# Kernel tuning notes

Measured on AMD Instinct MI355X. Metric: run time of the kernel, lower is better.

Reference implementation:

```python
import jax, jax.numpy as jnp
import numpy as np

N, H, W = 2, 96, 96
HL, WL = 48, 48
NCLS = 59


def _bn_params(key, c):
    k1, k2, k3, k4 = jax.random.split(key, 4)
    g = jax.random.uniform(k1, (c,), minval=0.5, maxval=1.5)
    b = jax.random.normal(k2, (c,)) * 0.1
    m = jax.random.normal(k3, (c,)) * 0.1
    v = jax.random.uniform(k4, (c,), minval=0.5, maxval=1.5)
    return jnp.stack([g, b, m, v])  # [4, C]


def _conv_w(key, shape):
    fan_in = shape[1] * shape[2] * shape[3]
    return jax.random.normal(key, shape) / np.sqrt(fan_in)


def setup_inputs() -> dict:
    key = jax.random.key(0)
    ks = jax.random.split(key, 32)
    return {
        "c1": jax.random.normal(ks[0], (N, 256, H, W)),
        "c2": jax.random.normal(ks[1], (N, 512, HL, WL)),
        "x": jax.random.normal(ks[2], (N, 2048, HL, WL)),
        "w_r1": _conv_w(ks[3], (64, 256, 3, 3)), "bn_r1": _bn_params(ks[4], 64),
        "w_r2": _conv_w(ks[5], (64, 64, 3, 3)), "bn_r2": _bn_params(ks[6], 64),
        "w_r3": _conv_w(ks[7], (64, 512, 1, 1)), "bn_r3": _bn_params(ks[8], 64),
        "w_p1": _conv_w(ks[9], (512, 2048, 1, 1)), "bn_p1": _bn_params(ks[10], 512),
        "w_p2": _conv_w(ks[11], (512, 2048, 1, 1)), "bn_p2": _bn_params(ks[12], 512),
        "w_p3": _conv_w(ks[13], (512, 2048, 1, 1)), "bn_p3": _bn_params(ks[14], 512),
        "w_p4": _conv_w(ks[15], (512, 2048, 1, 1)), "bn_p4": _bn_params(ks[16], 512),
        "w_c5": _conv_w(ks[17], (512, 4096, 3, 3)), "bn_c5": _bn_params(ks[18], 512),
        "w_c6": _conv_w(ks[19], (NCLS, 512, 1, 1)),
        "b_c6": jax.random.normal(ks[20], (NCLS,)) * 0.01,
    }


def conv2d(x, w, padding=0, dilation=1):
    return jax.lax.conv_general_dilated(
        x, w, window_strides=(1, 1), padding=[(padding, padding)] * 2,
        rhs_dilation=(dilation, dilation),
        dimension_numbers=("NCHW", "OIHW", "NCHW"))


def bn(x, p, eps=1e-5):
    g, b, m, v = p[0], p[1], p[2], p[3]
    scale = g * jax.lax.rsqrt(v + eps)
    return (x - m[None, :, None, None]) * scale[None, :, None, None] + b[None, :, None, None]


def resize_bilinear_ac(x, oh, ow):
    # bilinear, align_corners=True (matches torch interpolate)
    n, c, h, w = x.shape
    def coords(inp, out):
        if inp == 1 or out == 1:
            return jnp.zeros((out,), jnp.float32)
        return jnp.arange(out, dtype=jnp.float32) * ((inp - 1) / (out - 1))
    ys, xs = coords(h, oh), coords(w, ow)
    y0 = jnp.clip(jnp.floor(ys).astype(jnp.int32), 0, h - 1)
    y1 = jnp.clip(y0 + 1, 0, h - 1)
    wy = (ys - y0)[None, None, :, None]
    x0 = jnp.clip(jnp.floor(xs).astype(jnp.int32), 0, w - 1)
    x1 = jnp.clip(x0 + 1, 0, w - 1)
    wx = (xs - x0)[None, None, :]
    g = x[:, :, y0, :] * (1.0 - wy) + x[:, :, y1, :] * wy  # [n,c,oh,w]
    return g[:, :, :, x0] * (1.0 - wx[:, None]) + g[:, :, :, x1] * wx[:, None]


def unfold3x3_d2(x):
    # torch unfold(kernel=3, dilation=2, padding=2, stride=1) -> [n,c,9,h*w]
    n, c, h, w = x.shape
    p = jnp.pad(x, ((0, 0), (0, 0), (2, 2), (2, 2)))
    pats = jnp.stack([p[:, :, dy:dy + h, dx:dx + w]
                      for dy in (0, 2, 4) for dx in (0, 2, 4)], axis=2)
    return pats.reshape(n, c, 9, h * w)


def adaptive_avg_pool(x, s):
    n, c, h, w = x.shape  # h, w divisible by s here
    return x.reshape(n, c, s, h // s, s, w // s).mean(axis=(3, 5))


def reference(c1, c2, x, w_r1, bn_r1, w_r2, bn_r2, w_r3, bn_r3,
              w_p1, bn_p1, w_p2, bn_p2, w_p3, bn_p3, w_p4, bn_p4,
              w_c5, bn_c5, w_c6, b_c6):
    n, _, h, w = c1.shape
    # refine(c1): two dilated 3x3 convs -> query features [n,64,h,w]
    r = jax.nn.relu(bn(conv2d(c1, w_r1, padding=2, dilation=2), bn_r1))
    r = jax.nn.relu(bn(conv2d(r, w_r2, padding=2, dilation=2), bn_r2))
    # c2 -> upsample -> refine2 (1x1) -> key features [n,64,h,w]
    c2u = resize_bilinear_ac(c2, h, w)
    c2r = jax.nn.relu(bn(conv2d(c2u, w_r3), bn_r3))
    uc2 = unfold3x3_d2(c2r)                       # [n,64,9,hw]
    q = r.reshape(n, 64, h * w)                   # [n,64,hw]
    energy = jnp.einsum("ncp,nckp->npk", q, uc2)  # [n,hw,9]
    att = jax.nn.softmax(energy, axis=-1)
    # conv5 = PyramidPooling + 3x3 conv(4096->512) + BN + ReLU
    xh, xw = x.shape[2], x.shape[3]
    feats = [x]
    for s, wp, bnp in ((1, w_p1, bn_p1), (2, w_p2, bn_p2), (3, w_p3, bn_p3), (6, w_p4, bn_p4)):
        p = jax.nn.relu(bn(conv2d(adaptive_avg_pool(x, s), wp), bnp))
        feats.append(resize_bilinear_ac(p, xh, xw))
    psp = jnp.concatenate(feats, axis=1)          # [n,4096,xh,xw]
    out = jax.nn.relu(bn(conv2d(psp, w_c5, padding=1, dilation=1), bn_c5))  # [n,512,xh,xw]
    out0 = resize_bilinear_ac(out, h, w)          # [n,512,h,w]
    uo = unfold3x3_d2(out0)                       # [n,512,9,hw]
    agg = jnp.einsum("npk,nckp->ncp", att, uo).reshape(n, 512, h, w)
    # conv6: Dropout2d in eval mode = identity, then 1x1 conv with bias
    return conv2d(agg, w_c6) + b_c6[None, :, None, None]
```

## Files before the change

### kernel.cpp

```cpp
#include <hip/hip_runtime.h>
#include <hip/hip_bf16.h>
#include <cstddef>
#include <cstdint>

typedef __hip_bfloat16 hbf;
typedef __bf16 bf16x8 __attribute__((ext_vector_type(8)));
typedef __bf16 bf16x4 __attribute__((ext_vector_type(4)));
typedef float f32x4 __attribute__((ext_vector_type(4)));

#define GLDS(gp, lp) __builtin_amdgcn_global_load_lds( \
    (const __attribute__((address_space(1))) void*)(gp), \
    (__attribute__((address_space(3))) void*)(lp), 16, 0, 0)

__device__ __forceinline__ void bn_coef(const float* __restrict__ p, int C, int c,
                                        float& s, float& t) {
    float g = p[c];
    float b = p[C + c];
    float m = p[2 * C + c];
    float v = p[3 * C + c];
    s = g * rsqrtf(v + 1e-5f);
    t = b - m * s;
}

__global__ void k_fill0(uint32_t* __restrict__ p, int n) {
    int i = blockIdx.x * blockDim.x + threadIdx.x;
    if (i < n) p[i] = 0u;
}

__global__ __launch_bounds__(256) void k_c1trans(const float* __restrict__ x,
                                                 hbf* __restrict__ c1t) {
    __shared__ float tbuf[32][33];
    const int p0 = blockIdx.x * 32, c0 = blockIdx.y * 32, n = blockIdx.z;
    const int tx = threadIdx.x, ty = threadIdx.y;
#pragma unroll
    for (int i = 0; i < 4; ++i) {
        int ci = c0 + ty * 4 + i;
        tbuf[ty * 4 + i][tx] = x[((size_t)(n * 256 + ci)) * 9216 + p0 + tx];
    }
    __syncthreads();
#pragma unroll
    for (int i = 0; i < 4; ++i) {
        int p = p0 + ty * 4 + i;
        int pp = (p / 96 + 2) * 100 + (p % 96) + 2;
        c1t[((size_t)(n * 10000 + pp)) * 256 + c0 + tx] = __float2bfloat16(tbuf[tx][ty * 4 + i]);
    }
}

__global__ __launch_bounds__(256) void k_wsmall(const float* __restrict__ w1,
                                                hbf* __restrict__ wt1,
                                                const float* __restrict__ w2,
                                                hbf* __restrict__ wt2) {
    int b = blockIdx.x;
    if (b < 64) {
        int idx = b * 256 + threadIdx.x;
        int co = idx >> 8, ci = idx & 255;
        const float* s = w1 + ((size_t)(co * 256 + ci)) * 9;
#pragma unroll
        for (int tap = 0; tap < 9; ++tap)
            wt1[((size_t)(tap * 64 + co)) * 256 + ci] = __float2bfloat16(s[tap]);
    } else {
        int idx = (b - 64) * 256 + threadIdx.x;
        int co = idx >> 6, ci = idx & 63;
        const float* s = w2 + ((size_t)(co * 64 + ci)) * 9;
#pragma unroll
        for (int tap = 0; tap < 9; ++tap)
            wt2[((size_t)(tap * 64 + co)) * 64 + ci] = __float2bfloat16(s[tap]);
    }
}

template <int CI>
__global__ __launch_bounds__(256) void k_dconv_mfma(const hbf* __restrict__ wt,
                                                    const hbf* __restrict__ it,
                                                    float* __restrict__ accout) {
    __shared__ hbf As[2][3][64 * 32];
    __shared__ hbf Bs[2][140 * 32];
    const int tid = threadIdx.x;
    const int l = tid & 63, w = tid >> 6;
    const int P0 = blockIdx.x * 128;
    const int g  = blockIdx.y;
    const int r0 = tid >> 2;
    const int swzk = ((tid & 3) ^ ((r0 >> 1) & 3)) * 8;

    const int n_i = P0 / 9216;
    const int pl0 = P0 - n_i * 9216;
    const int pp0 = (pl0 / 96 + 2) * 100 + (pl0 % 96) + 2;
    const ptrdiff_t browbase = (ptrdiff_t)n_i * 10000 + pp0 + (g - 1) * 200 - 2;

    const int wn = w * 32;
    int jb[2];
#pragma unroll
    for (int tj = 0; tj < 2; ++tj) {
        int pl_lane = pl0 + wn + tj * 16 + (l & 15);
        jb[tj] = ((pl_lane / 96 + 2) * 100 + (pl_lane % 96) + 2) - pp0;
    }
    const int slotA = ((l >> 4) ^ ((l >> 1) & 3)) * 8;

    f32x4 acc[4][2];
#pragma unroll
    for (int i = 0; i < 4; ++i)
#pragma unroll
        for (int j = 0; j < 2; ++j) acc[i][j] = {0.f, 0.f, 0.f, 0.f};

    const hbf* gA = wt + ((size_t)(g * 192 + r0)) * CI + swzk;
    const hbf* gB = it + (size_t)(browbase + r0) * CI + swzk;

#define STAGE_D(buf, k0) do {                                                  \
        hbf* ldsA_ = &As[buf][0][0] + w * 512;                                 \
        hbf* ldsB_ = &Bs[buf][0] + w * 512;                                    \
        _Pragma("unroll")                                                      \
        for (int t_ = 0; t_ < 3; ++t_)                                         \
            GLDS(gA + (size_t)t_ * 64 * CI + (k0), ldsA_ + t_ * 2048);         \
        GLDS(gB + (k0), ldsB_);                                                \
        GLDS(gB + (size_t)64 * CI + (k0), ldsB_ + 2048);                       \
        if (tid < 48)                                                          \
            GLDS(gB + (size_t)128 * CI + (k0), &Bs[buf][0] + 4096);            \
    } while (0)

    STAGE_D(0, 0);
    int cur = 0;
#pragma unroll 2
    for (int k0 = 0; k0 < CI; k0 += 32) {
        __syncthreads();
        if (k0 + 32 < CI) STAGE_D(cur ^ 1, k0 + 32);
#pragma unroll
        for (int t = 0; t < 3; ++t) {
            bf16x8 af[4], bfr[2];
#pragma unroll
            for (int ti = 0; ti < 4; ++ti)
                af[ti] = *(const bf16x8*)(&As[cur][t][(ti * 16 + (l & 15)) * 32 + slotA]);
#pragma unroll
            for (int tj = 0; tj < 2; ++tj) {
                const int brow = jb[tj] + 2 * t;
                bfr[tj] = *(const bf16x8*)(&Bs[cur][0] + brow * 32 + (((l >> 4) ^ ((brow >> 1) & 3)) * 8));
            }
#pragma unroll
            for (int ti = 0; ti < 4; ++ti)
#pragma unroll
                for (int tj = 0; tj < 2; ++tj)
                    acc[ti][tj] = __builtin_amdgcn_mfma_f32_16x16x32_bf16(
                        af[ti], bfr[tj], acc[ti][tj], 0, 0, 0);
        }
        cur ^= 1;
    }
#undef STAGE_D

#pragma unroll
    for (int ti = 0; ti < 4; ++ti) {
        const int mrow = ti * 16 + (l >> 4) * 4;
#pragma unroll
        for (int tj = 0; tj < 2; ++tj) {
            const int px = P0 + wn + tj * 16 + (l & 15);
            const int n2 = px / 9216, pl2 = px % 9216;
            float* dst = accout + ((size_t)(n2 * 64 + mrow)) * 9216 + pl2;
#pragma unroll
            for (int r = 0; r < 4; ++r)
                atomicAdd(dst + (size_t)r * 9216, acc[ti][tj][r]);
        }
    }
}

__global__ __launch_bounds__(256) void k_ep_r1(const float* __restrict__ acc,
                                               const float* __restrict__ bnp,
                                               hbf* __restrict__ r1t) {
    const int q = threadIdx.x >> 6;
    const int ln = threadIdx.x & 63;
    const int pi = blockIdx.x * 64 + ln;
    const int n = pi / 9216, pl = pi % 9216;
    const int pp = (pl / 96 + 2) * 100 + (pl % 96) + 2;
    hbf* dst = r1t + ((size_t)(n * 10000 + pp)) * 64 + q * 16;
    const float* src = acc + (size_t)(n * 64 + q * 16) * 9216 + pl;
#pragma unroll
    for (int i = 0; i < 16; ++i) {
        float s, t; bn_coef(bnp, 64, q * 16 + i, s, t);
        dst[i] = __float2bfloat16(fmaxf(fmaf(src[(size_t)i * 9216], s, t), 0.f));
    }
}

__global__ __launch_bounds__(192) void k_conv1x1_c2(const float* __restrict__ c2,
                                                    const float* __restrict__ w,
                                                    float* __restrict__ outacc) {
    const int x = threadIdx.x;
    const int y = blockIdx.y * 4 + threadIdx.y;
    const int n = blockIdx.z >> 2;
    const int ci0 = (blockIdx.z & 3) * 128;
    const int cg = blockIdx.x;
    const int p = y * 48 + x;
    float acc[8];
#pragma unroll
    for (int j = 0; j < 8; ++j) acc[j] = 0.f;
    for (int ci = ci0; ci < ci0 + 128; ++ci) {
        float iv = c2[(size_t)(n * 512 + ci) * 2304 + p];
#pragma unroll
        for (int j = 0; j < 8; ++j)
            acc[j] = fmaf(iv, w[(size_t)(cg * 8 + j) * 512 + ci], acc[j]);
    }
#pragma unroll
    for (int j = 0; j < 8; ++j)
        atomicAdd(&outacc[(size_t)(n * 64 + cg * 8 + j) * 2304 + p], acc[j]);
}

__global__ void k_up96(const float* __restrict__ src, float* __restrict__ dst,
                       int C, const float* __restrict__ bnp) {
    int idx = blockIdx.x * blockDim.x + threadIdx.x;
    int p = idx % 9216;
    int nc = idx / 9216;
    int c = nc % C;
    int y = p / 96, x = p % 96;
    int yn = y * 47, xn = x * 47;
    int y0 = yn / 95, x0 = xn / 95;
    float wy = (float)(yn - y0 * 95) * (1.f / 95.f);
    float wx = (float)(xn - x0 * 95) * (1.f / 95.f);
    int y1 = min(y0 + 1, 47), x1 = min(x0 + 1, 47);
    const float* sp = src + (size_t)nc * 2304;
    float v00 = sp[y0 * 48 + x0], v01 = sp[y0 * 48 + x1];
    float v10 = sp[y1 * 48 + x0], v11 = sp[y1 * 48 + x1];
    float v = (v00 * (1.f - wx) + v01 * wx) * (1.f - wy)
            + (v10 * (1.f - wx) + v11 * wx) * wy;
    if (bnp) {
        float s, t; bn_coef(bnp, C, c, s, t);
        v = fmaxf(fmaf(v, s, t), 0.f);
    }
    dst[idx] = v;
}

__global__ __launch_bounds__(256) void k_attention(const float* __restrict__ qa,
                                                   const float* __restrict__ bnp,
                                                   const float* __restrict__ kf,
                                                   float* __restrict__ att) {
    const int wv = threadIdx.x >> 6;
    const int ln = threadIdx.x & 63;
    const int p_abs = blockIdx.x * 64 + ln;
    const int n = p_abs / 9216, p = p_abs % 9216;
    const int y = p / 96, x = p % 96;
    const float* qb = qa + ((size_t)(n * 64 + wv * 16)) * 9216 + p;
    float qv[16];
#pragma unroll
    for (int c = 0; c < 16; ++c) {
        float s, t; bn_coef(bnp, 64, wv * 16 + c, s, t);
        qv[c] = fmaxf(fmaf(qb[(size_t)c * 9216], s, t), 0.f);
    }
    const float* kb = kf + ((size_t)(n * 64 + wv * 16)) * 9216;
    float e[9];
#pragma unroll
    for (int ky = 0; ky < 3; ++ky)
#pragma unroll
        for (int kx = 0; kx < 3; ++kx) {
            int yy = y + 2 * ky - 2, xx = x + 2 * kx - 2;
            float s = 0.f;
            if (yy >= 0 && yy < 96 && xx >= 0 && xx < 96) {
                const float* kp = kb + yy * 96 + xx;
#pragma unroll
                for (int c = 0; c < 16; ++c) s = fmaf(qv[c], kp[(size_t)c * 9216], s);
            }
            e[ky * 3 + kx] = s;
        }
    __shared__ float pe[9][4][64];
#pragma unroll
    for (int k = 0; k < 9; ++k) pe[k][wv][ln] = e[k];
    __syncthreads();
    if (threadIdx.x < 64) {
        float ee[9];
#pragma unroll
        for (int k = 0; k < 9; ++k)
            ee[k] = (pe[k][0][ln] + pe[k][1][ln]) + (pe[k][2][ln] + pe[k][3][ln]);
        float m = ee[0];
#pragma unroll
        for (int k = 1; k < 9; ++k) m = fmaxf(m, ee[k]);
        float sum = 0.f;
#pragma unroll
        for (int k = 0; k < 9; ++k) { ee[k] = __expf(ee[k] - m); sum += ee[k]; }
        float inv = 1.f / sum;
        float* ap = att + (size_t)p_abs * 9;
#pragma unroll
        for (int k = 0; k < 9; ++k) ap[k] = ee[k] * inv;
    }
}

__global__ __launch_bounds__(64) void k_pool(const float* __restrict__ xin,
                                             float* __restrict__ pooled) {
    int b = blockIdx.x;
    int t = threadIdx.x;
    __shared__ float cells[50];
    if (t < 50) cells[t] = 0.f;
    __syncthreads();
    float rs = 0.f;
    if (t < 48) {
        const f32x4* rowv = (const f32x4*)(xin + (size_t)b * 2304 + t * 48);
        float s6[6];
#pragma unroll
        for (int j = 0; j < 6; ++j) {
            f32x4 u = rowv[2 * j], v = rowv[2 * j + 1];
            s6[j] = ((u[0] + u[1]) + (u[2] + u[3])) + ((v[0] + v[1]) + (v[2] + v[3]));
        }
        float s3a = s6[0] + s6[1], s3b = s6[2] + s6[3], s3c = s6[4] + s6[5];
        float s2a = s3a + s6[2], s2b = s6[3] + s3c;
        rs = s2a + s2b;
        int r6 = t >> 3, r3 = t >> 4, r2 = t / 24;
        atomicAdd(&cells[14 + r6 * 6 + 0], s6[0]);
        atomicAdd(&cells[14 + r6 * 6 + 1], s6[1]);
        atomicAdd(&cells[14 + r6 * 6 + 2], s6[2]);
        atomicAdd(&cells[14 + r6 * 6 + 3], s6[3]);
        atomicAdd(&cells[14 + r6 * 6 + 4], s6[4]);
        atomicAdd(&cells[14 + r6 * 6 + 5], s6[5]);
        atomicAdd(&cells[5 + r3 * 3 + 0], s3a);
        atomicAdd(&cells[5 + r3 * 3 + 1], s3b);
        atomicAdd(&cells[5 + r3 * 3 + 2], s3c);
        atomicAdd(&cells[1 + r2 * 2 + 0], s2a);
        atomicAdd(&cells[1 + r2 * 2 + 1], s2b);
    }
#pragma unroll
    for (int off = 32; off > 0; off >>= 1) rs += __shfl_down(rs, off);
    if (t == 0) atomicAdd(&cells[0], rs);
    __syncthreads();
    if (t < 50) {
        float inv = (t == 0) ? (1.f / 2304.f)
                  : (t < 5)  ? (1.f / 576.f)
                  : (t < 14) ? (1.f / 256.f)
                             : (1.f / 64.f);
        pooled[((size_t)(b >> 11) * 50 + t) * 2048 + (b & 2047)] = cells[t] * inv;
    }
}

__global__ __launch_bounds__(64) void k_pconv2(const float* __restrict__ pooled_t,
        const float* __restrict__ wp1, const float* __restrict__ bn1,
        const float* __restrict__ wp2, const float* __restrict__ bn2,
        const float* __restrict__ wp3, const float* __restrict__ bn3,
        const float* __restrict__ wp4, const float* __restrict__ bn4,
        float* __restrict__ pconv) {
    const int co = blockIdx.x, n = blockIdx.y;
    const int t = threadIdx.x;
    const int cell = (t < 50) ? t : 49;
    const float* w; const float* bnp;
    if (cell == 0)      { w = wp1; bnp = bn1; }
    else if (cell < 5)  { w = wp2; bnp = bn2; }
    else if (cell < 14) { w = wp3; bnp = bn3; }
    else                { w = wp4; bnp = bn4; }
    const float* pin = pooled_t + ((size_t)n * 50 + cell) * 2048;
    const float* wr = w + (size_t)co * 2048;
    float a0 = 0.f, a1 = 0.f, a2 = 0.f, a3 = 0.f;
    for (int c = 0; c < 2048; c += 4) {
        f32x4 v = *(const f32x4*)(pin + c);
        f32x4 ww = *(const f32x4*)(wr + c);
        a0 = fmaf(v[0], ww[0], a0);
        a1 = fmaf(v[1], ww[1], a1);
        a2 = fmaf(v[2], ww[2], a2);
        a3 = fmaf(v[3], ww[3], a3);
    }
    float a = (a0 + a1) + (a2 + a3);
    float s, tt; bn_coef(bnp, 512, co, s, tt);
    if (t < 50)
        pconv[((size_t)n * 512 + co) * 50 + cell] = fmaxf(fmaf(a, s, tt), 0.f);
}

__global__ __launch_bounds__(256) void k_wtrans_all(const float* __restrict__ w5,
                                                    hbf* __restrict__ wt,
                                                    hbf* __restrict__ wpsp) {
    int b = blockIdx.x;
    if (b < 4096) {
        int idx = b * 256 + threadIdx.x;
        int co = idx >> 11, ci = idx & 2047;
        const float* s = w5 + ((size_t)co * 4096 + ci) * 9;
#pragma unroll
        for (int tap = 0; tap < 9; ++tap)
            wt[((size_t)(tap * 512 + co)) * 2048 + ci] = __float2bfloat16(s[tap]);
    } else {
        int r = b - 4096;
        const int co = (r & 7) * 64 + (threadIdx.x & 63);
        const int bb = (r >> 3) & 3;
        const int c0 = (r >> 5) * 64 + (threadIdx.x >> 6) * 16;
        for (int i = 0; i < 16; ++i) {
            int c = c0 + i;
            const float* s = w5 + ((size_t)co * 4096 + 2048 + bb * 512 + c) * 9;
#pragma unroll
            for (int tap = 0; tap < 9; ++tap)
                wpsp[(((size_t)(tap * 4 + bb) * 512) + c) * 512 + co] = __float2bfloat16(s[tap]);
        }
    }
}

__global__ __launch_bounds__(64) void k_computeM2(const hbf* __restrict__ wpsp,
                                                  const float* __restrict__ pconv,
                                                  float* __restrict__ M) {
    const int cog = blockIdx.x, tap = blockIdx.y;
    const int n = blockIdx.z / 7, chunk = blockIdx.z % 7;
    const int cell0_t[7] = {0, 1, 5, 14, 23, 32, 41};
    const int ncell_t[7] = {1, 4, 9, 9, 9, 9, 9};
    const int btab[7]    = {0, 1, 2, 3, 3, 3, 3};
    const int cell0 = cell0_t[chunk], nc = ncell_t[chunk], b = btab[chunk];
    const int co = cog * 64 + threadIdx.x;
    const hbf* wb = wpsp + ((size_t)(tap * 4 + b) * 512) * 512 + co;
    const float* pc = pconv + (size_t)n * 512 * 50 + cell0;
    float acc[9];
#pragma unroll
    for (int j = 0; j < 9; ++j) acc[j] = 0.f;
    for (int c = 0; c < 512; ++c) {
        float w = __bfloat162float(wb[(size_t)c * 512]);
#pragma unroll
        for (int j = 0; j < 9; ++j)
            acc[j] = fmaf(w, pc[c * 50 + j], acc[j]);
    }
    float* Mp = M + ((size_t)(n * 512 + co) * 9 + tap) * 50 + cell0;
    for (int j = 0; j < nc; ++j) Mp[j] = acc[j];
}

struct B4 { int c0, c1, c2, c3; float w0, w1, w2, w3; };
__device__ __forceinline__ B4 cell_interp(int yy, int xx, int s, int base) {
    int sm1 = s - 1;
    int yn = yy * sm1, xn = xx * sm1;
    int y0 = yn / 47, x0 = xn / 47;
    float wy = (float)(yn - y0 * 47) * (1.f / 47.f);
    float wx = (float)(xn - x0 * 47) * (1.f / 47.f);
    int y1 = min(y0 + 1, sm1), x1 = min(x0 + 1, sm1);
    B4 r;
    r.c0 = base + y0 * s + x0; r.c1 = base + y0 * s + x1;
    r.c2 = base + y1 * s + x0; r.c3 = base + y1 * s + x1;
    r.w0 = (1.f - wy) * (1.f - wx); r.w1 = (1.f - wy) * wx;
    r.w2 = wy * (1.f - wx);         r.w3 = wy * wx;
    return r;
}

__global__ __launch_bounds__(256) void k_xtrans(const float* __restrict__ x,
                                                hbf* __restrict__ xtp) {
    __shared__ float tbuf[32][33];
    const int p0 = blockIdx.x * 32, c0 = blockIdx.y * 32, n = blockIdx.z;
    const int tx = threadIdx.x, ty = threadIdx.y;
#pragma unroll
    for (int i = 0; i < 4; ++i) {
        int ci = c0 + ty * 4 + i;
        tbuf[ty * 4 + i][tx] = x[((size_t)(n * 2048 + ci)) * 2304 + p0 + tx];
    }
    __syncthreads();
#pragma unroll
    for (int i = 0; i < 4; ++i) {
        int p = p0 + ty * 4 + i;
        int pp = (p / 48 + 1) * 50 + (p % 48) + 1;
        xtp[((size_t)(n * 2500 + pp)) * 2048 + c0 + tx] = __float2bfloat16(tbuf[tx][ty * 4 + i]);
    }
}

__global__ __launch_bounds__(256) void k_conv5_mfma(const hbf* __restrict__ wt,
                                                    const hbf* __restrict__ xtp,
                                                    float* __restrict__ c5acc) {
    __shared__ hbf As[2][3][128 * 32];
    __shared__ hbf Bs[2][136 * 32];
    const int tid = threadIdx.x;
    const int l = tid & 63, w = tid >> 6;
    const int m0 = blockIdx.x * 128;
    const int P0 = blockIdx.y * 128;
    const int g  = blockIdx.z;
    const int n_img = P0 / 2304;
    const int pbase = P0 - n_img * 2304;
    const int r0 = tid >> 2;
    const int swzk = ((tid & 3) ^ ((r0 >> 1) & 3)) * 8;

    const int pp0 = pbase + 2 * (pbase / 48) + 51;
    const ptrdiff_t browbase = (ptrdiff_t)n_img * 2500 + pp0 + (g - 1) * 50 - 1;

    const int wm = (w & 1) * 64, wn = (w >> 1) * 64;
    int jb[4];
#pragma unroll
    for (int tj = 0; tj < 4; ++tj) {
        int p = pbase + wn + tj * 16 + (l & 15);
        jb[tj] = p + 2 * (p / 48) + 51 - pp0;
    }
    const int slotA = ((l >> 4) ^ ((l >> 1) & 3)) * 8;

    f32x4 acc[4][4];
#pragma unroll
    for (int i = 0; i < 4; ++i)
#pragma unroll
        for (int j = 0; j < 4; ++j) acc[i][j] = {0.f, 0.f, 0.f, 0.f};

    const hbf* gA = wt + ((size_t)(g * 1536 + m0 + r0)) * 2048 + swzk;
    const hbf* gB = xtp + (size_t)(browbase + r0) * 2048 + swzk;

#define STAGE5(buf, k0) do {                                                       \
        hbf* ldsA_ = &As[buf][0][0] + w * 512;                                     \
        hbf* ldsB_ = &Bs[buf][0] + w * 512;                                        \
        _Pragma("unroll")                                                          \
        for (int t_ = 0; t_ < 3; ++t_) {                                           \
            GLDS(gA + (size_t)t_ * 512 * 2048 + (k0),             ldsA_ + t_ * 4096);      \
            GLDS(gA + (size_t)t_ * 512 * 2048 + 64 * 2048 + (k0), ldsA_ + t_ * 4096 + 2048); \
        }                                                                          \
        GLDS(gB + (k0),                      ldsB_);                               \
        GLDS(gB + (size_t)64 * 2048 + (k0),  ldsB_ + 2048);                        \
        if (tid < 32)                                                              \
            GLDS(gB + (size_t)128 * 2048 + (k0), &Bs[buf][0] + 4096);              \
    } while (0)

    STAGE5(0, 0);
    int cur = 0;
#pragma unroll 2
    for (int k0 = 0; k0 < 2048; k0 += 32) {
        __syncthreads();
        if (k0 + 32 < 2048) STAGE5(cur ^ 1, k0 + 32);
#pragma unroll
        for (int t = 0; t < 3; ++t) {
            bf16x8 af[4], bfr[4];
#pragma unroll
            for (int ti = 0; ti < 4; ++ti)
                af[ti] = *(const bf16x8*)(&As[cur][t][(wm + ti * 16 + (l & 15)) * 32 + slotA]);
#pragma unroll
            for (int tj = 0; tj < 4; ++tj) {
                const int brow = jb[tj] + t;
                bfr[tj] = *(const bf16x8*)(&Bs[cur][0] + brow * 32 + (((l >> 4) ^ ((brow >> 1) & 3)) * 8));
            }
#pragma unroll
            for (int ti = 0; ti < 4; ++ti)
#pragma unroll
                for (int tj = 0; tj < 4; ++tj)
                    acc[ti][tj] = __builtin_amdgcn_mfma_f32_16x16x32_bf16(
                        af[ti], bfr[tj], acc[ti][tj], 0, 0, 0);
        }
        cur ^= 1;
    }
#undef STAGE5

#pragma unroll
    for (int ti = 0; ti < 4; ++ti) {
        const int mrow = wm + ti * 16 + (l >> 4) * 4;
#pragma unroll
        for (int tj = 0; tj < 4; ++tj) {
            const int p = pbase + wn + tj * 16 + (l & 15);
            float* dst = c5acc + ((size_t)(n_img * 512 + m0 + mrow)) * 2304 + p;
#pragma unroll
            for (int r = 0; r < 4; ++r)
                atomicAdd(dst + (size_t)r * 2304, acc[ti][tj][r]);
        }
    }
}

__global__ __launch_bounds__(256) void k_bnrelu_psp(const float* __restrict__ c5acc,
                                                    const float* __restrict__ M,
                                                    const float* __restrict__ bnp,
                                                    hbf* __restrict__ c5out) {
    const int co = blockIdx.x, n = blockIdx.y;
    __shared__ float Ms[450];
    const float* Mrow = M + ((size_t)(n * 512 + co)) * 450;
    for (int i = threadIdx.x; i < 450; i += 256) Ms[i] = Mrow[i];
    __syncthreads();
    float s, t; bn_coef(bnp, 512, co, s, t);
    const size_t base = ((size_t)(n * 512 + co)) * 2304;
#pragma unroll
    for (int i = 0; i < 9; ++i) {
        int p = threadIdx.x + i * 256;
        int y = p / 48, x = p % 48;
        float a = c5acc[base + p];
#pragma unroll
        for (int ky = 0; ky < 3; ++ky) {
            int yy = y + ky - 1;
            if (yy < 0 || yy > 47) continue;
#pragma unroll
            for (int kx = 0; kx < 3; ++kx) {
                int xx = x + kx - 1;
                if (xx < 0 || xx > 47) continue;
                const float* Mp = Ms + (ky * 3 + kx) * 50;
                float sa = Mp[0];
                B4 b2 = cell_interp(yy, xx, 2, 1);
                B4 b3 = cell_interp(yy, xx, 3, 5);
                B4 b6 = cell_interp(yy, xx, 6, 14);
                sa = fmaf(b2.w0, Mp[b2.c0], sa); sa = fmaf(b2.w1, Mp[b2.c1], sa);
                sa = fmaf(b2.w2, Mp[b2.c2], sa); sa = fmaf(b2.w3, Mp[b2.c3], sa);
                sa = fmaf(b3.w0, Mp[b3.c0], sa); sa = fmaf(b3.w1, Mp[b3.c1], sa);
                sa = fmaf(b3.w2, Mp[b3.c2], sa); sa = fmaf(b3.w3, Mp[b3.c3], sa);
                sa = fmaf(b6.w0, Mp[b6.c0], sa); sa = fmaf(b6.w1, Mp[b6.c1], sa);
                sa = fmaf(b6.w2, Mp[b6.c2], sa); sa = fmaf(b6.w3, Mp[b6.c3], sa);
                a += sa;
            }
        }
        c5out[base + p] = __float2bfloat16(fmaxf(fmaf(a, s, t), 0.f));
    }
}

__global__ __launch_bounds__(192) void k_conv6s(const hbf* __restrict__ c5o,
                                                const float* __restrict__ w,
                                                float* __restrict__ out) {
    const int x = threadIdx.x;
    const int y = blockIdx.y * 4 + threadIdx.y;
    const int n = blockIdx.z;
    const int co = blockIdx.x;
    const int p = y * 48 + x;
    const hbf* ip = c5o + (size_t)n * 512 * 2304 + p;
    const float* wr = w + (size_t)co * 512;
    float a0 = 0.f, a1 = 0.f, a2 = 0.f, a3 = 0.f;
    for (int ci = 0; ci < 512; ci += 4) {
        a0 = fmaf(__bfloat162float(ip[(size_t)ci * 2304]),       wr[ci],     a0);
        a1 = fmaf(__bfloat162float(ip[(size_t)(ci + 1) * 2304]), wr[ci + 1], a1);
        a2 = fmaf(__bfloat162float(ip[(size_t)(ci + 2) * 2304]), wr[ci + 2], a2);
        a3 = fmaf(__bfloat162float(ip[(size_t)(ci + 3) * 2304]), wr[ci + 3], a3);
    }
    out[((size_t)n * 59 + co) * 2304 + p] = (a0 + a1) + (a2 + a3);
}

__global__ void k_final(const float* __restrict__ att, const float* __restrict__ c6s,
                        const float* __restrict__ bias, float* __restrict__ out) {
    int idx = blockIdx.x * blockDim.x + threadIdx.x;
    int p = idx % 9216;
    int nc = idx / 9216;
    int cls = nc % 59, n = nc / 59;
    int y = p / 96, x = p % 96;
    const float* ar = att + ((size_t)n * 9216 + p) * 9;
    const float* cp = c6s + (size_t)nc * 2304;
    int xs0[3], xs1[3], ys0[3], ys1[3];
    float fx[3], fy[3];
#pragma unroll
    for (int d = 0; d < 3; ++d) {
        int xx = x + 2 * d - 2;
        if (xx >= 0 && xx < 96) {
            int xn = xx * 47, x0 = xn / 95;
            xs0[d] = x0; xs1[d] = min(x0 + 1, 47);
            fx[d] = (float)(xn - x0 * 95) * (1.f / 95.f);
        } else { xs0[d] = -1; xs1[d] = 0; fx[d] = 0.f; }
        int yy = y + 2 * d - 2;
        if (yy >= 0 && yy < 96) {
            int yn = yy * 47, y0 = yn / 95;
            ys0[d] = y0; ys1[d] = min(y0 + 1, 47);
            fy[d] = (float)(yn - y0 * 95) * (1.f / 95.f);
        } else { ys0[d] = -1; ys1[d] = 0; fy[d] = 0.f; }
    }
    float a = bias[cls];
#pragma unroll
    for (int ky = 0; ky < 3; ++ky) {
        if (ys0[ky] < 0) continue;
        const float* r0 = cp + ys0[ky] * 48;
        const float* r1 = cp + ys1[ky] * 48;
        float wy = fy[ky];
#pragma unroll
        for (int kx = 0; kx < 3; ++kx) {
            if (xs0[kx] < 0) continue;
            float wx = fx[kx];
            float v0 = r0[xs0[kx]] * (1.f - wx) + r0[xs1[kx]] * wx;
            float v1 = r1[xs0[kx]] * (1.f - wx) + r1[xs1[kx]] * wx;
            a = fmaf(ar[ky * 3 + kx], v0 * (1.f - wy) + v1 * wy, a);
        }
    }
    out[idx] = a;
}

extern "C" void kernel_launch(void* const* d_in, const int* in_sizes, int n_in,
                              void* d_out, int out_size, void* d_ws, size_t ws_size,
                              hipStream_t stream) {
    const float* c1    = (const float*)d_in[0];
    const float* c2    = (const float*)d_in[1];
    const float* xin   = (const float*)d_in[2];
    const float* w_r1  = (const float*)d_in[3];
    const float* bn_r1 = (const float*)d_in[4];
    const float* w_r2  = (const float*)d_in[5];
    const float* bn_r2 = (const float*)d_in[6];
    const float* w_r3  = (const float*)d_in[7];
    const float* bn_r3 = (const float*)d_in[8];
    const float* w_p1  = (const float*)d_in[9];
    const float* bn_p1 = (const float*)d_in[10];
    const float* w_p2  = (const float*)d_in[11];
    const float* bn_p2 = (const float*)d_in[12];
    const float* w_p3  = (const float*)d_in[13];
    const float* bn_p3 = (const float*)d_in[14];
    const float* w_p4  = (const float*)d_in[15];
    const float* bn_p4 = (const float*)d_in[16];
    const float* w_c5  = (const float*)d_in[17];
    const float* bn_c5 = (const float*)d_in[18];
    const float* w_c6  = (const float*)d_in[19];
    const float* b_c6  = (const float*)d_in[20];
    float* out = (float*)d_out;
    (void)in_sizes; (void)n_in; (void)out_size; (void)ws_size;

    char* base = (char*)d_ws;
    float* att = (float*)base;
    char*  A   = base + 663552;
    hbf*   c1t   = (hbf*)A;
    hbf*   r1t   = (hbf*)(A + 10240000);
    float* r1acc = (float*)(A + 12800000);
    float* qacc  = (float*)(A + 17518592);
    float* c2acc = (float*)(A + 22237184);
    float* c2r   = (float*)(A + 28135424);
    hbf*   wr1t  = (hbf*)(A + 32854016);
    hbf*   wr2t  = (hbf*)(A + 33148928);
    hbf*   wpsp   = (hbf*)A;
    float* pooled = (float*)(A + 48791552);
    float* pconv  = (float*)(A + 49610752);
    float* M      = (float*)(A + 49815552);
    hbf*   xtp    = (hbf*)A;
    float* c5acc  = (float*)(A + 20480000);
    hbf*   wt     = (hbf*)(A + 29917184);
    hbf*   c5out = (hbf*)A;
    float* c6s   = (float*)(A + 4718592);

    k_fill0<<<dim3(22868), 256, 0, stream>>>((uint32_t*)A, 5854208);
    k_c1trans<<<dim3(288, 8, 2), dim3(32, 8), 0, stream>>>(c1, c1t);
    k_wsmall<<<dim3(80), 256, 0, stream>>>(w_r1, wr1t, w_r2, wr2t);
    k_dconv_mfma<256><<<dim3(144, 3), 256, 0, stream>>>(wr1t, c1t, r1acc);
    k_ep_r1<<<dim3(288), 256, 0, stream>>>(r1acc, bn_r1, r1t);
    k_dconv_mfma<64><<<dim3(144, 3), 256, 0, stream>>>(wr2t, r1t, qacc);
    k_conv1x1_c2<<<dim3(8, 12, 8), dim3(48, 4), 0, stream>>>(c2, w_r3, c2acc);
    k_up96<<<dim3(2 * 64 * 9216 / 256), 256, 0, stream>>>(c2acc, c2r, 64, bn_r3);
    k_attention<<<dim3(288), 256, 0, stream>>>(qacc, bn_r2, c2r, att);
    k_pool<<<dim3(4096), 64, 0, stream>>>(xin, pooled);
    k_pconv2<<<dim3(512, 2), 64, 0, stream>>>(pooled, w_p1, bn_p1, w_p2, bn_p2,
                                              w_p3, bn_p3, w_p4, bn_p4, pconv);
    k_wtrans_all<<<dim3(4352), 256, 0, stream>>>(w_c5, wt, wpsp);
    k_computeM2<<<dim3(8, 9, 14), 64, 0, stream>>>(wpsp, pconv, M);
    k_fill0<<<dim3(29216), 256, 0, stream>>>((uint32_t*)xtp, 7479296);
    k_xtrans<<<dim3(72, 64, 2), dim3(32, 8), 0, stream>>>(xin, xtp);
    k_conv5_mfma<<<dim3(4, 36, 3), 256, 0, stream>>>(wt, xtp, c5acc);
    k_bnrelu_psp<<<dim3(512, 2), 256, 0, stream>>>(c5acc, M, bn_c5, c5out);
    k_conv6s<<<dim3(59, 12, 2), dim3(48, 4), 0, stream>>>(c5out, w_c6, c6s);
    k_final<<<dim3(2 * 59 * 9216 / 256), 256, 0, stream>>>(att, c6s, b_c6, out);
}
```

Measured before the change: 661.7 us.

## Drop atomics in dilated conv and transpose attention inputs to pixel-major

The dilated 3x3 conv kernel now loops over all three kernel-row groups inside one block with 64-pixel tiles, so it writes results directly instead of accumulating through atomics. The zero-fill region shrinks to match. Two new transpose kernels apply BN/ReLU (and the bilinear upsample for the key features) and store q and k as pixel-major [p,64], so the attention kernel can use vectorized float4 loads instead of channel-strided ones. The c2 1x1 conv now computes 16 output channels per thread. The costs are two extra small kernels and a dconv grid with fewer blocks but longer serial K loops.

```diff
diff --git a/kernel.cpp b/kernel.cpp
--- a/kernel.cpp
+++ b/kernel.cpp
@@ -5,7 +5,6 @@
 
 typedef __hip_bfloat16 hbf;
 typedef __bf16 bf16x8 __attribute__((ext_vector_type(8)));
-typedef __bf16 bf16x4 __attribute__((ext_vector_type(4)));
 typedef float f32x4 __attribute__((ext_vector_type(4)));
 
 #define GLDS(gp, lp) __builtin_amdgcn_global_load_lds( \
@@ -72,90 +71,74 @@
 __global__ __launch_bounds__(256) void k_dconv_mfma(const hbf* __restrict__ wt,
                                                     const hbf* __restrict__ it,
                                                     float* __restrict__ accout) {
+    constexpr int KS = CI / 32;
     __shared__ hbf As[2][3][64 * 32];
-    __shared__ hbf Bs[2][140 * 32];
+    __shared__ hbf Bs[2][72 * 32];
     const int tid = threadIdx.x;
     const int l = tid & 63, w = tid >> 6;
-    const int P0 = blockIdx.x * 128;
-    const int g  = blockIdx.y;
+    const int P0 = blockIdx.x * 64;
     const int r0 = tid >> 2;
     const int swzk = ((tid & 3) ^ ((r0 >> 1) & 3)) * 8;
 
     const int n_i = P0 / 9216;
     const int pl0 = P0 - n_i * 9216;
     const int pp0 = (pl0 / 96 + 2) * 100 + (pl0 % 96) + 2;
-    const ptrdiff_t browbase = (ptrdiff_t)n_i * 10000 + pp0 + (g - 1) * 200 - 2;
-
-    const int wn = w * 32;
-    int jb[2];
-#pragma unroll
-    for (int tj = 0; tj < 2; ++tj) {
-        int pl_lane = pl0 + wn + tj * 16 + (l & 15);
-        jb[tj] = ((pl_lane / 96 + 2) * 100 + (pl_lane % 96) + 2) - pp0;
-    }
+    const ptrdiff_t bb0 = (ptrdiff_t)n_i * 10000 + pp0 - 202;
+
+    const int wn = w * 16;
+    const int pl_lane = pl0 + wn + (l & 15);
+    const int jb = ((pl_lane / 96 + 2) * 100 + (pl_lane % 96) + 2) - pp0;
     const int slotA = ((l >> 4) ^ ((l >> 1) & 3)) * 8;
 
-    f32x4 acc[4][2];
-#pragma unroll
-    for (int i = 0; i < 4; ++i)
-#pragma unroll
-        for (int j = 0; j < 2; ++j) acc[i][j] = {0.f, 0.f, 0.f, 0.f};
-
-    const hbf* gA = wt + ((size_t)(g * 192 + r0)) * CI + swzk;
-    const hbf* gB = it + (size_t)(browbase + r0) * CI + swzk;
-
-#define STAGE_D(buf, k0) do {                                                  \
+    f32x4 acc[4];
+#pragma unroll
+    for (int i = 0; i < 4; ++i) acc[i] = {0.f, 0.f, 0.f, 0.f};
+
+#define STAGE_D(buf, gg, k0) do {                                              \
+        const hbf* gA_ = wt + ((size_t)((gg) * 192 + r0)) * CI + swzk;         \
+        const hbf* gB_ = it + (size_t)(bb0 + (gg) * 200 + r0) * CI + swzk;     \
         hbf* ldsA_ = &As[buf][0][0] + w * 512;                                 \
         hbf* ldsB_ = &Bs[buf][0] + w * 512;                                    \
         _Pragma("unroll")                                                      \
         for (int t_ = 0; t_ < 3; ++t_)                                         \
-            GLDS(gA + (size_t)t_ * 64 * CI + (k0), ldsA_ + t_ * 2048);         \
-        GLDS(gB + (k0), ldsB_);                                                \
-        GLDS(gB + (size_t)64 * CI + (k0), ldsB_ + 2048);                       \
-        if (tid < 48)                                                          \
-            GLDS(gB + (size_t)128 * CI + (k0), &Bs[buf][0] + 4096);            \
+            GLDS(gA_ + (size_t)t_ * 64 * CI + (k0), ldsA_ + t_ * 2048);        \
+        GLDS(gB_ + (k0), ldsB_);                                               \
+        if (tid < 32)                                                          \
+            GLDS(gB_ + (size_t)64 * CI + (k0), &Bs[buf][0] + 2048);            \
     } while (0)
 
-    STAGE_D(0, 0);
+    STAGE_D(0, 0, 0);
     int cur = 0;
-#pragma unroll 2
-    for (int k0 = 0; k0 < CI; k0 += 32) {
-        __syncthreads();
-        if (k0 + 32 < CI) STAGE_D(cur ^ 1, k0 + 32);
-#pragma unroll
-        for (int t = 0; t < 3; ++t) {
-            bf16x8 af[4], bfr[2];
-#pragma unroll
-            for (int ti = 0; ti < 4; ++ti)
-                af[ti] = *(const bf16x8*)(&As[cur][t][(ti * 16 + (l & 15)) * 32 + slotA]);
-#pragma unroll
-            for (int tj = 0; tj < 2; ++tj) {
-                const int brow = jb[tj] + 2 * t;
-                bfr[tj] = *(const bf16x8*)(&Bs[cur][0] + brow * 32 + (((l >> 4) ^ ((brow >> 1) & 3)) * 8));
+    for (int g = 0; g < 3; ++g) {
+#pragma unroll
+        for (int ks = 0; ks < KS; ++ks) {
+            __syncthreads();
+            int ns = g * KS + ks + 1;
+            if (ns < 3 * KS) STAGE_D(cur ^ 1, ns / KS, (ns % KS) * 32);
+#pragma unroll
+            for (int t = 0; t < 3; ++t) {
+                const int brow = jb + 2 * t;
+                bf16x8 bfr = *(const bf16x8*)(&Bs[cur][0] + brow * 32 + (((l >> 4) ^ ((brow >> 1) & 3)) * 8));
+#pragma unroll
+                for (int ti = 0; ti < 4; ++ti) {
+                    bf16x8 af = *(const bf16x8*)(&As[cur][t][(ti * 16 + (l & 15)) * 32 + slotA]);
+                    acc[ti] = __builtin_amdgcn_mfma_f32_16x16x32_bf16(af, bfr, acc[ti], 0, 0, 0);
+                }
             }
-#pragma unroll
-            for (int ti = 0; ti < 4; ++ti)
-#pragma unroll
-                for (int tj = 0; tj < 2; ++tj)
-                    acc[ti][tj] = __builtin_amdgcn_mfma_f32_16x16x32_bf16(
-                        af[ti], bfr[tj], acc[ti][tj], 0, 0, 0);
-        }
-        cur ^= 1;
+            cur ^= 1;
+        }
     }
 #undef STAGE_D
 
+    const int px = P0 + wn + (l & 15);
+    const int n2 = px / 9216, pl2 = px % 9216;
 #pragma unroll
     for (int ti = 0; ti < 4; ++ti) {
         const int mrow = ti * 16 + (l >> 4) * 4;
-#pragma unroll
-        for (int tj = 0; tj < 2; ++tj) {
-            const int px = P0 + wn + tj * 16 + (l & 15);
-            const int n2 = px / 9216, pl2 = px % 9216;
-            float* dst = accout + ((size_t)(n2 * 64 + mrow)) * 9216 + pl2;
-#pragma unroll
-            for (int r = 0; r < 4; ++r)
-                atomicAdd(dst + (size_t)r * 9216, acc[ti][tj][r]);
-        }
+        float* dst = accout + ((size_t)(n2 * 64 + mrow)) * 9216 + pl2;
+#pragma unroll
+        for (int r = 0; r < 4; ++r)
+            dst[(size_t)r * 9216] = acc[ti][r];
     }
 }
 
@@ -176,6 +159,59 @@
     }
 }
 
+__global__ __launch_bounds__(256) void k_qt(const float* __restrict__ acc,
+                                            const float* __restrict__ bnp,
+                                            float* __restrict__ qt) {
+    __shared__ float tbuf[32][33];
+    const int p0 = blockIdx.x * 32, c0 = blockIdx.y * 32, n = blockIdx.z;
+    const int tx = threadIdx.x, ty = threadIdx.y;
+#pragma unroll
+    for (int i = 0; i < 4; ++i) {
+        int ci = c0 + ty * 4 + i;
+        tbuf[ty * 4 + i][tx] = acc[((size_t)(n * 64 + ci)) * 9216 + p0 + tx];
+    }
+    __syncthreads();
+    float s, t; bn_coef(bnp, 64, c0 + tx, s, t);
+#pragma unroll
+    for (int i = 0; i < 4; ++i) {
+        int p = p0 + ty * 4 + i;
+        qt[((size_t)(n * 9216 + p)) * 64 + c0 + tx] =
+            fmaxf(fmaf(tbuf[tx][ty * 4 + i], s, t), 0.f);
+    }
+}
+
+__global__ __launch_bounds__(256) void k_kt(const float* __restrict__ c2acc,
+                                            const float* __restrict__ bnp,
+                                            float* __restrict__ kt) {
+    __shared__ float tbuf[32][33];
+    const int p0 = blockIdx.x * 32, c0 = blockIdx.y * 32, n = blockIdx.z;
+    const int tx = threadIdx.x, ty = threadIdx.y;
+    const int p = p0 + tx;
+    const int y = p / 96, x = p % 96;
+    int yn = y * 47, xn = x * 47;
+    int y0 = yn / 95, x0 = xn / 95;
+    float wy = (float)(yn - y0 * 95) * (1.f / 95.f);
+    float wx = (float)(xn - x0 * 95) * (1.f / 95.f);
+    int y1 = min(y0 + 1, 47), x1 = min(x0 + 1, 47);
+#pragma unroll
+    for (int i = 0; i < 4; ++i) {
+        int c = c0 + ty * 4 + i;
+        const float* sp = c2acc + ((size_t)(n * 64 + c)) * 2304;
+        float v00 = sp[y0 * 48 + x0], v01 = sp[y0 * 48 + x1];
+        float v10 = sp[y1 * 48 + x0], v11 = sp[y1 * 48 + x1];
+        tbuf[ty * 4 + i][tx] = (v00 * (1.f - wx) + v01 * wx) * (1.f - wy)
+                             + (v10 * (1.f - wx) + v11 * wx) * wy;
+    }
+    __syncthreads();
+    float s, t; bn_coef(bnp, 64, c0 + tx, s, t);
+#pragma unroll
+    for (int i = 0; i < 4; ++i) {
+        int pw = p0 + ty * 4 + i;
+        kt[((size_t)(n * 9216 + pw)) * 64 + c0 + tx] =
+            fmaxf(fmaf(tbuf[tx][ty * 4 + i], s, t), 0.f);
+    }
+}
+
 __global__ __launch_bounds__(192) void k_conv1x1_c2(const float* __restrict__ c2,
                                                     const float* __restrict__ w,
                                                     float* __restrict__ outacc) {
@@ -185,61 +221,39 @@
     const int ci0 = (blockIdx.z & 3) * 128;
     const int cg = blockIdx.x;
     const int p = y * 48 + x;
-    float acc[8];
-#pragma unroll
-    for (int j = 0; j < 8; ++j) acc[j] = 0.f;
+    float acc[16];
+#pragma unroll
+    for (int j = 0; j < 16; ++j) acc[j] = 0.f;
     for (int ci = ci0; ci < ci0 + 128; ++ci) {
         float iv = c2[(size_t)(n * 512 + ci) * 2304 + p];
 #pragma unroll
-        for (int j = 0; j < 8; ++j)
-            acc[j] = fmaf(iv, w[(size_t)(cg * 8 + j) * 512 + ci], acc[j]);
-    }
-#pragma unroll
-    for (int j = 0; j < 8; ++j)
-        atomicAdd(&outacc[(size_t)(n * 64 + cg * 8 + j) * 2304 + p], acc[j]);
-}
-
-__global__ void k_up96(const float* __restrict__ src, float* __restrict__ dst,
-                       int C, const float* __restrict__ bnp) {
-    int idx = blockIdx.x * blockDim.x + threadIdx.x;
-    int p = idx % 9216;
-    int nc = idx / 9216;
-    int c = nc % C;
-    int y = p / 96, x = p % 96;
-    int yn = y * 47, xn = x * 47;
-    int y0 = yn / 95, x0 = xn / 95;
-    float wy = (float)(yn - y0 * 95) * (1.f / 95.f);
-    float wx = (float)(xn - x0 * 95) * (1.f / 95.f);
-    int y1 = min(y0 + 1, 47), x1 = min(x0 + 1, 47);
-    const float* sp = src + (size_t)nc * 2304;
-    float v00 = sp[y0 * 48 + x0], v01 = sp[y0 * 48 + x1];
-    float v10 = sp[y1 * 48 + x0], v11 = sp[y1 * 48 + x1];
-    float v = (v00 * (1.f - wx) + v01 * wx) * (1.f - wy)
-            + (v10 * (1.f - wx) + v11 * wx) * wy;
-    if (bnp) {
-        float s, t; bn_coef(bnp, C, c, s, t);
-        v = fmaxf(fmaf(v, s, t), 0.f);
-    }
-    dst[idx] = v;
-}
-
-__global__ __launch_bounds__(256) void k_attention(const float* __restrict__ qa,
-                                                   const float* __restrict__ bnp,
-                                                   const float* __restrict__ kf,
+        for (int j = 0; j < 16; ++j)
+            acc[j] = fmaf(iv, w[(size_t)(cg * 16 + j) * 512 + ci], acc[j]);
+    }
+#pragma unroll
+    for (int j = 0; j < 16; ++j)
+        atomicAdd(&outacc[(size_t)(n * 64 + cg * 16 + j) * 2304 + p], acc[j]);
+}
+
+__global__ __launch_bounds__(256) void k_attention(const float* __restrict__ qt,
+                                                   const float* __restrict__ kt,
                                                    float* __restrict__ att) {
     const int wv = threadIdx.x >> 6;
     const int ln = threadIdx.x & 63;
     const int p_abs = blockIdx.x * 64 + ln;
     const int n = p_abs / 9216, p = p_abs % 9216;
     const int y = p / 96, x = p % 96;
-    const float* qb = qa + ((size_t)(n * 64 + wv * 16)) * 9216 + p;
     float qv[16];
-#pragma unroll
-    for (int c = 0; c < 16; ++c) {
-        float s, t; bn_coef(bnp, 64, wv * 16 + c, s, t);
-        qv[c] = fmaxf(fmaf(qb[(size_t)c * 9216], s, t), 0.f);
-    }
-    const float* kb = kf + ((size_t)(n * 64 + wv * 16)) * 9216;
+    {
+        const f32x4* qr = (const f32x4*)(qt + (size_t)p_abs * 64 + wv * 16);
+#pragma unroll
+        for (int j = 0; j < 4; ++j) {
+            f32x4 v = qr[j];
+            qv[4 * j + 0] = v[0]; qv[4 * j + 1] = v[1];
+            qv[4 * j + 2] = v[2]; qv[4 * j + 3] = v[3];
+        }
+    }
+    const float* kb = kt + (size_t)n * 9216 * 64 + wv * 16;
     float e[9];
 #pragma unroll
     for (int ky = 0; ky < 3; ++ky)
@@ -248,9 +262,15 @@
             int yy = y + 2 * ky - 2, xx = x + 2 * kx - 2;
             float s = 0.f;
             if (yy >= 0 && yy < 96 && xx >= 0 && xx < 96) {
-                const float* kp = kb + yy * 96 + xx;
-#pragma unroll
-                for (int c = 0; c < 16; ++c) s = fmaf(qv[c], kp[(size_t)c * 9216], s);
+                const f32x4* kr = (const f32x4*)(kb + (size_t)(yy * 96 + xx) * 64);
+#pragma unroll
+                for (int j = 0; j < 4; ++j) {
+                    f32x4 kv = kr[j];
+                    s = fmaf(qv[4 * j + 0], kv[0], s);
+                    s = fmaf(qv[4 * j + 1], kv[1], s);
+                    s = fmaf(qv[4 * j + 2], kv[2], s);
+                    s = fmaf(qv[4 * j + 3], kv[3], s);
+                }
             }
             e[ky * 3 + kx] = s;
         }
@@ -669,10 +689,11 @@
     char*  A   = base + 663552;
     hbf*   c1t   = (hbf*)A;
     hbf*   r1t   = (hbf*)(A + 10240000);
-    float* r1acc = (float*)(A + 12800000);
-    float* qacc  = (float*)(A + 17518592);
-    float* c2acc = (float*)(A + 22237184);
-    float* c2r   = (float*)(A + 28135424);
+    float* c2acc = (float*)(A + 12800000);
+    float* r1acc = (float*)(A + 13979648);
+    float* qacc  = (float*)(A + 18698240);
+    float* q_t   = (float*)(A + 23416832);
+    float* k_t   = (float*)(A + 28135424);
     hbf*   wr1t  = (hbf*)(A + 32854016);
     hbf*   wr2t  = (hbf*)(A + 33148928);
     hbf*   wpsp   = (hbf*)A;
@@ -685,15 +706,16 @@
     hbf*   c5out = (hbf*)A;
     float* c6s   = (float*)(A + 4718592);
 
-    k_fill0<<<dim3(22868), 256, 0, stream>>>((uint32_t*)A, 5854208);
+    k_fill0<<<dim3(13652), 256, 0, stream>>>((uint32_t*)A, 3494912);
     k_c1trans<<<dim3(288, 8, 2), dim3(32, 8), 0, stream>>>(c1, c1t);
     k_wsmall<<<dim3(80), 256, 0, stream>>>(w_r1, wr1t, w_r2, wr2t);
-    k_dconv_mfma<256><<<dim3(144, 3), 256, 0, stream>>>(wr1t, c1t, r1acc);
+    k_dconv_mfma<256><<<dim3(288), 256, 0, stream>>>(wr1t, c1t, r1acc);
     k_ep_r1<<<dim3(288), 256, 0, stream>>>(r1acc, bn_r1, r1t);
-    k_dconv_mfma<64><<<dim3(144, 3), 256, 0, stream>>>(wr2t, r1t, qacc);
-    k_conv1x1_c2<<<dim3(8, 12, 8), dim3(48, 4), 0, stream>>>(c2, w_r3, c2acc);
-    k_up96<<<dim3(2 * 64 * 9216 / 256), 256, 0, stream>>>(c2acc, c2r, 64, bn_r3);
-    k_attention<<<dim3(288), 256, 0, stream>>>(qacc, bn_r2, c2r, att);
+    k_dconv_mfma<64><<<dim3(288), 256, 0, stream>>>(wr2t, r1t, qacc);
+    k_qt<<<dim3(288, 2, 2), dim3(32, 8), 0, stream>>>(qacc, bn_r2, q_t);
+    k_conv1x1_c2<<<dim3(4, 12, 8), dim3(48, 4), 0, stream>>>(c2, w_r3, c2acc);
+    k_kt<<<dim3(288, 2, 2), dim3(32, 8), 0, stream>>>(c2acc, bn_r3, k_t);
+    k_attention<<<dim3(288), 256, 0, stream>>>(q_t, k_t, att);
     k_pool<<<dim3(4096), 64, 0, stream>>>(xin, pooled);
     k_pconv2<<<dim3(512, 2), 64, 0, stream>>>(pooled, w_p1, bn_p1, w_p2, bn_p2,
                                               w_p3, bn_p3, w_p4, bn_p4, pconv);
```

Result: no change. 653.3 us (-1.3%).
